# Kernel optimization log

Measured on AMD Instinct MI355X. Metric: run time of the kernel, lower is better.

## Reference

```python
import jax, jax.numpy as jnp
import numpy as np

B, S, DM, H, DH = 2, 2048, 2048, 8, 128
INNER = H * DH
ROPE_BASE = 10000.0


def setup_inputs() -> dict:
    key = jax.random.key(0)
    ks = jax.random.split(key, 8)
    sc = 0.02
    return {
        "x": jax.random.normal(ks[0], (B, S, DM), jnp.float32),
        "Wq": jax.random.normal(ks[1], (INNER, DM), jnp.float32) * sc,
        "Wk": jax.random.normal(ks[2], (INNER, DM), jnp.float32) * sc,
        "Wv": jax.random.normal(ks[3], (INNER, DM), jnp.float32) * sc,
        "Wo": jax.random.normal(ks[4], (DM, INNER), jnp.float32) * sc,
        "Wb": jax.random.normal(ks[5], (H, DM), jnp.float32) * sc,
        "bb": jax.random.normal(ks[6], (H,), jnp.float32) * sc,
        "alpha_log": -2.0 + 0.5 * jax.random.normal(ks[7], (H, DH), jnp.float32),
    }


def _rope(t):
    # cos/sin tables of shape [S, DH//2]
    inv_freq = 1.0 / (ROPE_BASE ** (jnp.arange(0, DH, 2, dtype=jnp.float32) / DH))
    freqs = jnp.arange(t, dtype=jnp.float32)[:, None] * inv_freq[None, :]
    return jnp.cos(freqs), jnp.sin(freqs)


def _apply_rotary(x, cos, sin):
    # x: [B,S,H,DH]; cos/sin: [S, DH//2] broadcast over B,H
    x1, x2 = x[..., : DH // 2], x[..., DH // 2 :]
    c = cos[None, :, None, :]
    s = sin[None, :, None, :]
    return jnp.concatenate([x1 * c - x2 * s, x2 * c + x1 * s], axis=-1)


def reference(x, Wq, Wk, Wv, Wo, Wb, bb, alpha_log):
    q = (x @ Wq.T).reshape(B, S, H, DH)
    k = (x @ Wk.T).reshape(B, S, H, DH)
    v = (x @ Wv.T).reshape(B, S, H, DH)

    cos, sin = _rope(S)
    q = _apply_rotary(q, cos, sin)
    k = _apply_rotary(k, cos, sin)

    alpha = jax.nn.sigmoid(alpha_log)                 # [H, DH]
    beta = jax.nn.sigmoid(x @ Wb.T + bb)              # [B, S, H]

    # parallel path: decayed causal linear attention
    qk = jnp.einsum("bshd,bthd->bhst", q, k)          # [B,H,S,S]
    alpha_mean = alpha.mean(axis=-1)                  # [H]
    log_alpha = jnp.log(jnp.clip(alpha_mean, 1e-6))
    pos = jnp.arange(S, dtype=jnp.float32)
    td = pos[:, None] - pos[None, :]                  # [S,S]
    decay_exp = td[None, :, :] * log_alpha[:, None, None]
    decay_exp = jnp.where(td[None, :, :] < 0, -jnp.inf, decay_exp)
    decay = jnp.exp(decay_exp)                        # [B? no: H,S,S]
    weights = qk * decay[None] * beta.transpose(0, 2, 1)[:, :, None, :]
    out = jnp.einsum("bhst,bthe->bshe", weights, v)   # [B,S,H,DH]
    output = out.reshape(B, S, INNER) @ Wo.T          # [B,S,DM]

    # accumulated state (no-grad in original): recurrent scan over time
    alpha_b = alpha[None, :, :, None]                 # [1,H,DH,1]
    kT = jnp.transpose(k, (1, 0, 2, 3))               # [S,B,H,DH]
    vT = jnp.transpose(v, (1, 0, 2, 3))
    bT = jnp.transpose(beta, (1, 0, 2))               # [S,B,H]

    def step(state, inp):
        k_t, v_t, b_t = inp
        kv = jnp.einsum("bhd,bhe->bhde", k_t, v_t)
        state = alpha_b * state + b_t[:, :, None, None] * kv
        return state, None

    state0 = jnp.zeros((B, H, DH, DH), jnp.float32)
    state, _ = jax.lax.scan(step, state0, (kT, vT, bT))
    return output, state
```

## Files before the change

kernel.cpp:

```cpp
#include <hip/hip_runtime.h>
#include <hip/hip_bf16.h>
#include <cstdint>
#include <cstddef>

#define S_LEN 2048
#define DMODEL 2048
#define NHEADS 8
#define DHEAD 128
#define INNER_DIM 1024
#define BATCH 2

typedef __bf16 bf16;
typedef __bf16 bf16x8 __attribute__((ext_vector_type(8)));
typedef __bf16 bf16x4 __attribute__((ext_vector_type(4)));
typedef float f32x4 __attribute__((ext_vector_type(4)));

#define VMCNT(n) asm volatile("s_waitcnt vmcnt(" #n ")" ::: "memory")
#define BAR()                                \
  do {                                       \
    asm volatile("" ::: "memory");           \
    __builtin_amdgcn_s_barrier();            \
    asm volatile("" ::: "memory");           \
  } while (0)

__device__ __forceinline__ void gload_lds16(const void* g, void* l) {
  __builtin_amdgcn_global_load_lds(
      (const __attribute__((address_space(1))) void*)g,
      (__attribute__((address_space(3))) void*)l, 16, 0, 0);
}

__device__ __forceinline__ float sigmoidf_(float x) {
  return 1.0f / (1.0f + expf(-x));
}

__global__ __launch_bounds__(256) void convert_w_kernel(
    const float* __restrict__ wq, const float* __restrict__ wk,
    const float* __restrict__ wv, const float* __restrict__ wo,
    bf16* __restrict__ wqkvb, bf16* __restrict__ wob) {
  size_t i4 = ((size_t)blockIdx.x * 256 + threadIdx.x) * 4;
  const float* src;
  bf16* dst;
  size_t off;
  if (i4 < 2097152UL)       { src = wq; dst = wqkvb;           off = i4; }
  else if (i4 < 4194304UL)  { src = wk; dst = wqkvb + 2097152; off = i4 - 2097152UL; }
  else if (i4 < 6291456UL)  { src = wv; dst = wqkvb + 4194304; off = i4 - 4194304UL; }
  else                      { src = wo; dst = wob;             off = i4 - 6291456UL; }
  float4 v = *(const float4*)(src + off);
  bf16x4 o;
  o[0] = (bf16)v.x; o[1] = (bf16)v.y; o[2] = (bf16)v.z; o[3] = (bf16)v.w;
  *(bf16x4*)(dst + off) = o;
}

__global__ __launch_bounds__(64) void alpha_kernel(
    const float* __restrict__ alpha_log, float* __restrict__ la_mean,
    float* __restrict__ la_d) {
  int h = blockIdx.x;
  int lane = threadIdx.x;
  float a1 = sigmoidf_(alpha_log[h * 128 + lane]);
  float a2 = sigmoidf_(alpha_log[h * 128 + 64 + lane]);
  la_d[h * 128 + lane] = logf(a1);
  la_d[h * 128 + 64 + lane] = logf(a2);
  float s = a1 + a2;
  for (int off = 32; off; off >>= 1) s += __shfl_down(s, off);
  if (lane == 0) la_mean[h] = logf(fmaxf(s * (1.0f / 128.0f), 1e-6f));
}

__global__ __launch_bounds__(64) void beta_xb_kernel(
    const float* __restrict__ x, const float* __restrict__ Wb,
    const float* __restrict__ bbias, float* __restrict__ beta,
    bf16* __restrict__ xb) {
  int n = blockIdx.x;
  int lane = threadIdx.x;
  float acc[8];
#pragma unroll
  for (int h = 0; h < 8; h++) acc[h] = 0.0f;
  const float4* x4 = (const float4*)(x + (size_t)n * DMODEL);
  bf16* xbr = xb + (size_t)n * DMODEL;
  for (int d4 = lane; d4 < DMODEL / 4; d4 += 64) {
    float4 xv = x4[d4];
    bf16x4 o;
    o[0] = (bf16)xv.x; o[1] = (bf16)xv.y; o[2] = (bf16)xv.z; o[3] = (bf16)xv.w;
    *(bf16x4*)(xbr + d4 * 4) = o;
#pragma unroll
    for (int h = 0; h < 8; h++) {
      float4 wv = ((const float4*)(Wb + (size_t)h * DMODEL))[d4];
      acc[h] += xv.x * wv.x + xv.y * wv.y + xv.z * wv.z + xv.w * wv.w;
    }
  }
#pragma unroll
  for (int off = 32; off; off >>= 1)
#pragma unroll
    for (int h = 0; h < 8; h++) acc[h] += __shfl_down(acc[h], off);
  if (lane == 0) {
#pragma unroll
    for (int h = 0; h < 8; h++)
      beta[(size_t)n * 8 + h] = sigmoidf_(acc[h] + bbias[h]);
  }
}

#define QKV_K 2048
#define QKV_NT 32

__global__ __launch_bounds__(512, 2) void qkv_gemm8p_kernel(
    const bf16* __restrict__ A, const bf16* __restrict__ Bm,
    bf16* __restrict__ C, bf16* __restrict__ vt) {
  __shared__ __align__(16) bf16 smem[2][32768];

  const int id = blockIdx.x;
  const int wg = (id & 7) * 32 + (id >> 3);
  const int tile_n = (wg >> 5) * 384;
  const int tile_m = (wg & 31) * 128;

  const int tid = threadIdx.x;
  const int lane = tid & 63;
  const int w = tid >> 6;
  const int wm = w >> 2;
  const int wn = w & 3;
  const int lr = lane & 15;
  const int kq = lane >> 4;

  const int srow = lane >> 3;
  const int slot = lane & 7;
  const int sgo = (slot ^ srow) * 8;
  const int rloc = w * 8 + srow;

  size_t Aoff[2], Boff[6];
#pragma unroll
  for (int a = 0; a < 2; ++a)
    Aoff[a] = (size_t)(tile_m + a * 64 + rloc) * QKV_K + sgo;
#pragma unroll
  for (int b = 0; b < 6; ++b) {
    const int ldsr = b * 64 + rloc;
    const int qn = ldsr >= 192 ? 1 : 0;
    const int rem = ldsr - qn * 192;
    const int wng = rem / 48;
    const int rr = rem - wng * 48;
    const int gcol = wng * 96 + qn * 48 + rr;
    Boff[b] = (size_t)(tile_n + gcol) * QKV_K + sgo;
  }

  f32x4 acc[4][6];
#pragma unroll
  for (int i = 0; i < 4; i++)
#pragma unroll
    for (int j = 0; j < 6; j++) acc[i][j] = (f32x4){0.f, 0.f, 0.f, 0.f};

  auto stageAA = [&](int buf, int k0) {
#pragma unroll
    for (int a = 0; a < 2; ++a)
      gload_lds16(A + Aoff[a] + k0, &smem[buf][(a * 64 + w * 8) * 64]);
  };
  auto stageB2 = [&](int buf, int k0, int b0) {
#pragma unroll
    for (int u = 0; u < 2; ++u)
      gload_lds16(Bm + Boff[b0 + u] + k0,
                  &smem[buf][8192 + ((b0 + u) * 64 + w * 8) * 64]);
  };

  stageAA(0, 0);
  stageB2(0, 0, 0);
  stageB2(0, 0, 2);
  stageB2(0, 0, 4);
  stageAA(1, 64);
  VMCNT(5);
  BAR();

  for (int t = 0; t < QKV_NT; ++t) {
    const int buf = t & 1;
    const int k0n = (t + 1) * 64;
    const bool h1 = (t + 1 < QKV_NT);
    const bool h2 = (t + 2 < QKV_NT);
    const bf16* ldsA = smem[buf];
    const bf16* ldsB = smem[buf] + 8192;

    bf16x8 af[2][2], b0f[3][2], b1f[3][2];

#pragma unroll
    for (int mi = 0; mi < 2; ++mi)
#pragma unroll
      for (int ks = 0; ks < 2; ++ks)
        af[mi][ks] = *(const bf16x8*)&ldsA[(wm * 64 + mi * 16 + lr) * 64 +
                                           (((ks * 4 + kq) ^ (lr & 7)) * 8)];
#pragma unroll
    for (int ni = 0; ni < 3; ++ni)
#pragma unroll
      for (int ks = 0; ks < 2; ++ks)
        b0f[ni][ks] = *(const bf16x8*)&ldsB[(wn * 48 + ni * 16 + lr) * 64 +
                                            (((ks * 4 + kq) ^ (lr & 7)) * 8)];
    if (h1) stageB2(buf ^ 1, k0n, 0);
    BAR();
    __builtin_amdgcn_s_setprio(1);
#pragma unroll
    for (int mi = 0; mi < 2; ++mi)
#pragma unroll
      for (int ni = 0; ni < 3; ++ni)
#pragma unroll
        for (int ks = 0; ks < 2; ++ks)
          acc[mi][ni] = __builtin_amdgcn_mfma_f32_16x16x32_bf16(
              af[mi][ks], b0f[ni][ks], acc[mi][ni], 0, 0, 0);
    __builtin_amdgcn_s_setprio(0);
    if (h1) VMCNT(4);
    else VMCNT(0);
    BAR();

#pragma unroll
    for (int ni = 0; ni < 3; ++ni)
#pragma unroll
      for (int ks = 0; ks < 2; ++ks)
        b1f[ni][ks] = *(const bf16x8*)&ldsB[(192 + wn * 48 + ni * 16 + lr) * 64 +
                                            (((ks * 4 + kq) ^ (lr & 7)) * 8)];
    if (h1) stageB2(buf ^ 1, k0n, 2);
    BAR();
    __builtin_amdgcn_s_setprio(1);
#pragma unroll
    for (int mi = 0; mi < 2; ++mi)
#pragma unroll
      for (int ni = 0; ni < 3; ++ni)
#pragma unroll
        for (int ks = 0; ks < 2; ++ks)
          acc[mi][3 + ni] = __builtin_amdgcn_mfma_f32_16x16x32_bf16(
              af[mi][ks], b1f[ni][ks], acc[mi][3 + ni], 0, 0, 0);
    __builtin_amdgcn_s_setprio(0);
    BAR();

#pragma unroll
    for (int mi = 0; mi < 2; ++mi)
#pragma unroll
      for (int ks = 0; ks < 2; ++ks)
        af[mi][ks] = *(const bf16x8*)&ldsA[(wm * 64 + 32 + mi * 16 + lr) * 64 +
                                           (((ks * 4 + kq) ^ (lr & 7)) * 8)];
    if (h1) stageB2(buf ^ 1, k0n, 4);
    BAR();
    __builtin_amdgcn_s_setprio(1);
#pragma unroll
    for (int mi = 0; mi < 2; ++mi)
#pragma unroll
      for (int ni = 0; ni < 3; ++ni)
#pragma unroll
        for (int ks = 0; ks < 2; ++ks)
          acc[2 + mi][3 + ni] = __builtin_amdgcn_mfma_f32_16x16x32_bf16(
              af[mi][ks], b1f[ni][ks], acc[2 + mi][3 + ni], 0, 0, 0);
    __builtin_amdgcn_s_setprio(0);
    BAR();

    if (h2) stageAA(buf, (t + 2) * 64);
    BAR();
    __builtin_amdgcn_s_setprio(1);
#pragma unroll
    for (int mi = 0; mi < 2; ++mi)
#pragma unroll
      for (int ni = 0; ni < 3; ++ni)
#pragma unroll
        for (int ks = 0; ks < 2; ++ks)
          acc[2 + mi][ni] = __builtin_amdgcn_mfma_f32_16x16x32_bf16(
              af[mi][ks], b0f[ni][ks], acc[2 + mi][ni], 0, 0, 0);
    __builtin_amdgcn_s_setprio(0);
    if (h1) {
      if (h2) VMCNT(5);
      else VMCNT(3);
    }
    BAR();
  }

  const int rb = kq * 4;
#pragma unroll
  for (int mi = 0; mi < 4; ++mi) {
    const int row0 = tile_m + wm * 64 + mi * 16 + rb;
#pragma unroll
    for (int ni = 0; ni < 6; ++ni) {
      const int col = tile_n + wn * 96 + ni * 16 + lr;
      const int z = col >> 10;
      const int cz = col & 1023;
      bf16* Cz = C + (size_t)z * 4194304UL;
#pragma unroll
      for (int r2 = 0; r2 < 4; ++r2)
        Cz[(size_t)(row0 + r2) * 1024 + cz] = (bf16)acc[mi][ni][r2];
      if (z == 2) {
        const int bb2 = row0 >> 11;
        const int ss = row0 & 2047;
        bf16x4 o4;
#pragma unroll
        for (int r2 = 0; r2 < 4; ++r2) o4[r2] = (bf16)acc[mi][ni][r2];
        *(bf16x4*)&vt[(((size_t)bb2 * 8 + (cz >> 7)) * 128 + (cz & 127)) * 2048 +
                      ss] = o4;
      }
    }
  }
}

__global__ __launch_bounds__(256) void gemm_bt_kernel(
    const bf16* __restrict__ A, const bf16* __restrict__ Bm, void* Cv, int K,
    int N, size_t strideB, size_t strideC, int obf, bf16* __restrict__ vt) {
  const int id = blockIdx.x + gridDim.x * (blockIdx.y + gridDim.y * blockIdx.z);
  const int xcd = id & 7;
  const int s = id >> 3;
  const int xs = gridDim.x >> 2;
  const int ys = gridDim.y >> 1;
  const int perz = xs * ys;
  const int z = s / perz;
  const int r = s - z * perz;
  const int tx = (xcd & 3) * xs + (r % xs);
  const int ty = (xcd >> 2) * ys + (r / xs);
  const int tile_n = tx * 128;
  const int tile_m = ty * 128;

  const bf16* Bp = Bm + (size_t)z * strideB;
  const int tid = threadIdx.x;
  const int lane = tid & 63;
  const int wv = tid >> 6;

  __shared__ bf16 As[128 * 32];
  __shared__ bf16 Bs[128 * 32];

  f32x4 acc[4][4];
#pragma unroll
  for (int i = 0; i < 4; i++)
#pragma unroll
    for (int j = 0; j < 4; j++) acc[i][j] = (f32x4){0.f, 0.f, 0.f, 0.f};

  const int wm = (wv >> 1) * 64;
  const int wn = (wv & 1) * 64;
  const int lr = lane & 15;
  const int kq = lane >> 4;
  const int swzA = ((wm + lr) >> 1) & 3;
  const int swzB = ((wn + lr) >> 1) & 3;
  const int kA = (kq ^ swzA) * 8;
  const int kB = (kq ^ swzB) * 8;

  const int ar = wv * 32 + (lane >> 2);
  const int g = ((lane & 3) ^ ((ar >> 1) & 3)) * 8;
  const bf16* Ag = A + (size_t)(tile_m + ar) * K + g;
  const bf16* Bg = Bp + (size_t)(tile_n + ar) * K + g;
  bf16* AsW = &As[wv * 1024];
  bf16* BsW = &Bs[wv * 1024];

  for (int k0 = 0; k0 < K; k0 += 32) {
    gload_lds16(Ag + k0, AsW);
    gload_lds16(Ag + (size_t)16 * K + k0, AsW + 512);
    gload_lds16(Bg + k0, BsW);
    gload_lds16(Bg + (size_t)16 * K + k0, BsW + 512);
    __syncthreads();
    bf16x8 af[4], bfr[4];
#pragma unroll
    for (int mi = 0; mi < 4; mi++)
      af[mi] = *(const bf16x8*)&As[(wm + mi * 16 + lr) * 32 + kA];
#pragma unroll
    for (int ni = 0; ni < 4; ni++)
      bfr[ni] = *(const bf16x8*)&Bs[(wn + ni * 16 + lr) * 32 + kB];
#pragma unroll
    for (int mi = 0; mi < 4; mi++)
#pragma unroll
      for (int ni = 0; ni < 4; ni++)
        acc[mi][ni] = __builtin_amdgcn_mfma_f32_16x16x32_bf16(
            af[mi], bfr[ni], acc[mi][ni], 0, 0, 0);
    __syncthreads();
  }

  const int crow0 = tile_m + wm + (lane >> 4) * 4;
  const int ccol = tile_n + wn + (lane & 15);
  if (obf) {
    bf16* Cb = (bf16*)Cv + (size_t)z * strideC;
#pragma unroll
    for (int mi = 0; mi < 4; mi++)
#pragma unroll
      for (int ni = 0; ni < 4; ni++)
#pragma unroll
        for (int r2 = 0; r2 < 4; r2++)
          Cb[(size_t)(crow0 + mi * 16 + r2) * N + ccol + ni * 16] =
              (bf16)acc[mi][ni][r2];
    if (z == 2) {
#pragma unroll
      for (int mi = 0; mi < 4; mi++) {
        int row0 = crow0 + mi * 16;
        int bb2 = row0 >> 11, ss = row0 & 2047;
#pragma unroll
        for (int ni = 0; ni < 4; ni++) {
          int col = ccol + ni * 16;
          bf16x4 o4;
#pragma unroll
          for (int r2 = 0; r2 < 4; r2++) o4[r2] = (bf16)acc[mi][ni][r2];
          *(bf16x4*)&vt[(((size_t)bb2 * 8 + (col >> 7)) * 128 + (col & 127)) *
                            2048 +
                        ss] = o4;
        }
      }
    }
  } else {
    float* Cf = (float*)Cv + (size_t)z * strideC;
#pragma unroll
    for (int mi = 0; mi < 4; mi++)
#pragma unroll
      for (int ni = 0; ni < 4; ni++)
#pragma unroll
        for (int r2 = 0; r2 < 4; r2++)
          Cf[(size_t)(crow0 + mi * 16 + r2) * N + ccol + ni * 16] =
              acc[mi][ni][r2];
  }
}

__global__ __launch_bounds__(256) void rope_kernel(bf16* __restrict__ q,
                                                   bf16* __restrict__ k) {
  int idx = blockIdx.x * 256 + threadIdx.x;
  int j0 = (idx & 15) * 4;
  int nh = idx >> 4;
  int s = (nh >> 3) & (S_LEN - 1);
  size_t base = (size_t)nh * 128 + j0;
  bf16x4 qa = *(bf16x4*)&q[base], qb = *(bf16x4*)&q[base + 64];
  bf16x4 ka = *(bf16x4*)&k[base], kb = *(bf16x4*)&k[base + 64];
#pragma unroll
  for (int jj = 0; jj < 4; jj++) {
    float inv = expf(-(float)(j0 + jj) * (9.210340371976184f / 64.0f));
    float f = (float)s * inv;
    float sn, c;
    sincosf(f, &sn, &c);
    float q1 = (float)qa[jj], q2 = (float)qb[jj];
    qa[jj] = (bf16)(q1 * c - q2 * sn);
    qb[jj] = (bf16)(q2 * c + q1 * sn);
    float k1 = (float)ka[jj], k2 = (float)kb[jj];
    ka[jj] = (bf16)(k1 * c - k2 * sn);
    kb[jj] = (bf16)(k2 * c + k1 * sn);
  }
  *(bf16x4*)&q[base] = qa;
  *(bf16x4*)&q[base + 64] = qb;
  *(bf16x4*)&k[base] = ka;
  *(bf16x4*)&k[base + 64] = kb;
}

__global__ __launch_bounds__(256) void attn_mfma_kernel(
    const bf16* __restrict__ q, const bf16* __restrict__ k,
    const bf16* __restrict__ vt, const float* __restrict__ beta,
    const float* __restrict__ la_mean, bf16* __restrict__ outb) {
  const int s0 = blockIdx.x * 64;
  const int h = blockIdx.y;
  const int b = blockIdx.z;
  const int tid = threadIdx.x;
  const int w = tid >> 6;
  const int lane = tid & 63;
  const int lr = lane & 15;
  const int kq = lane >> 4;
  const float la = la_mean[h];

  __shared__ __align__(16) bf16 Ps[4][2][16][72];

  const int sg = s0 + w * 16;
  const size_t qbase =
      ((size_t)b * S_LEN + (sg + lr)) * INNER_DIM + h * 128 + kq * 8;
  bf16x8 aq[4];
#pragma unroll
  for (int ks = 0; ks < 4; ks++)
    aq[ks] = *(const bf16x8*)&q[qbase + ks * 32];

  f32x4 O[8];
#pragma unroll
  for (int en = 0; en < 8; en++) O[en] = (f32x4){0.f, 0.f, 0.f, 0.f};

  const size_t kbase = (size_t)b * S_LEN * INNER_DIM + h * 128 + kq * 8;
  const size_t vtbase = ((size_t)b * 8 + h) * 128 * 2048;

#pragma unroll
  for (int tile = 0; tile < 2; tile++) {
    const int tb = s0 - 64 + tile * 64;
    f32x4 sc[4];
#pragma unroll
    for (int nt = 0; nt < 4; nt++) sc[nt] = (f32x4){0.f, 0.f, 0.f, 0.f};
#pragma unroll
    for (int nt = 0; nt < 4; nt++) {
      int t = tb + nt * 16 + lr;
      int tc = t > 0 ? t : 0;
#pragma unroll
      for (int ks = 0; ks < 4; ks++) {
        bf16x8 bk = *(const bf16x8*)&k[kbase + (size_t)tc * INNER_DIM + ks * 32];
        sc[nt] = __builtin_amdgcn_mfma_f32_16x16x32_bf16(aq[ks], bk, sc[nt],
                                                         0, 0, 0);
      }
    }
#pragma unroll
    for (int nt = 0; nt < 4; nt++) {
      int t = tb + nt * 16 + lr;
      int tc = t > 0 ? t : 0;
      float bt = beta[((size_t)b * S_LEN + tc) * 8 + h];
#pragma unroll
      for (int reg = 0; reg < 4; reg++) {
        int qrow = sg + kq * 4 + reg;
        int td = qrow - t;
        float wgt = 0.0f;
        if (t >= 0 && td >= 0 && td < 64)
          wgt = sc[nt][reg] * __expf((float)td * la) * bt;
        Ps[w][tile][kq * 4 + reg][nt * 16 + lr] = (bf16)wgt;
      }
    }
    __syncthreads();
    bf16x8 ap[2];
#pragma unroll
    for (int ks2 = 0; ks2 < 2; ks2++)
      ap[ks2] = *(const bf16x8*)&Ps[w][tile][lr][ks2 * 32 + kq * 8];
#pragma unroll
    for (int en = 0; en < 8; en++) {
#pragma unroll
      for (int ks2 = 0; ks2 < 2; ks2++) {
        int t0f = tb + ks2 * 32 + kq * 8;
        int tcf = t0f > 0 ? t0f : 0;
        bf16x8 bv = *(const bf16x8*)&vt[vtbase + (size_t)(en * 16 + lr) * 2048 +
                                        tcf];
        O[en] = __builtin_amdgcn_mfma_f32_16x16x32_bf16(ap[ks2], bv, O[en], 0,
                                                        0, 0);
      }
    }
  }
  const size_t obase = (size_t)b * S_LEN * INNER_DIM + h * 128;
#pragma unroll
  for (int en = 0; en < 8; en++) {
#pragma unroll
    for (int reg = 0; reg < 4; reg++) {
      int qrow = sg + kq * 4 + reg;
      outb[obase + (size_t)qrow * INNER_DIM + en * 16 + lr] =
          (bf16)O[en][reg];
    }
  }
}

__global__ __launch_bounds__(256) void state_partial_kernel(
    const bf16* __restrict__ k, const bf16* __restrict__ v,
    const float* __restrict__ beta, const float* __restrict__ la_d,
    float* __restrict__ part) {
  const int bh = blockIdx.x;
  const int chunk = blockIdx.y;
  const int b = bh >> 3, h = bh & 7;
  const int t0 = S_LEN - 512 + chunk * 32;
  const int tid = threadIdx.x;
  const int d = tid >> 1;
  const int eh = (tid & 1) * 64;

  __shared__ float ks[32][128];
  __shared__ float vsm[32][128];
  __shared__ float bs[32];

  const size_t bh_off = ((size_t)b * S_LEN) * INNER_DIM + (size_t)h * 128;
  for (int u = tid; u < 32 * 16; u += 256) {
    int r = u >> 4, c8 = (u & 15) * 8;
    bf16x8 kv = *(const bf16x8*)&k[bh_off + (size_t)(t0 + r) * INNER_DIM + c8];
    bf16x8 vv = *(const bf16x8*)&v[bh_off + (size_t)(t0 + r) * INNER_DIM + c8];
#pragma unroll
    for (int j = 0; j < 8; j++) {
      ks[r][c8 + j] = (float)kv[j];
      vsm[r][c8 + j] = (float)vv[j];
    }
  }
  if (tid < 32) bs[tid] = beta[((size_t)b * S_LEN + t0 + tid) * 8 + h];
  __syncthreads();

  const float lad = la_d[h * 128 + d];
  float acc[64];
#pragma unroll
  for (int e = 0; e < 64; e++) acc[e] = 0.0f;

  for (int tl = 0; tl < 32; tl++) {
    int m = (S_LEN - 1) - (t0 + tl);
    float f = __expf((float)m * lad);
    float coef = bs[tl] * ks[tl][d] * f;
    if (coef != 0.0f) {
#pragma unroll
      for (int e = 0; e < 64; e += 4) {
        float4 vv = *(const float4*)&vsm[tl][eh + e];
        acc[e + 0] = fmaf(coef, vv.x, acc[e + 0]);
        acc[e + 1] = fmaf(coef, vv.y, acc[e + 1]);
        acc[e + 2] = fmaf(coef, vv.z, acc[e + 2]);
        acc[e + 3] = fmaf(coef, vv.w, acc[e + 3]);
      }
    }
  }
  float* pp = part + (((size_t)chunk * 16 + bh) * 16384 + (size_t)d * 128 + eh);
#pragma unroll
  for (int e = 0; e < 64; e += 4) {
    float4 o = {acc[e + 0], acc[e + 1], acc[e + 2], acc[e + 3]};
    *(float4*)&pp[e] = o;
  }
}

__global__ __launch_bounds__(256) void state_reduce_kernel(
    const float* __restrict__ part, float* __restrict__ state) {
  size_t off = ((size_t)blockIdx.x * 256 + threadIdx.x) * 4;
  float4 s = {0.f, 0.f, 0.f, 0.f};
#pragma unroll
  for (int c = 0; c < 16; c++) {
    float4 p = *(const float4*)&part[(size_t)c * 262144 + off];
    s.x += p.x; s.y += p.y; s.z += p.z; s.w += p.w;
  }
  *(float4*)&state[off] = s;
}

extern "C" void kernel_launch(void* const* d_in, const int* in_sizes, int n_in,
                              void* d_out, int out_size, void* d_ws,
                              size_t ws_size, hipStream_t stream) {
  const float* x = (const float*)d_in[0];
  const float* Wq = (const float*)d_in[1];
  const float* Wk = (const float*)d_in[2];
  const float* Wv = (const float*)d_in[3];
  const float* Wo = (const float*)d_in[4];
  const float* Wb = (const float*)d_in[5];
  const float* bb = (const float*)d_in[6];
  const float* alog = (const float*)d_in[7];
  float* out = (float*)d_out;

  char* ws = (char*)d_ws;
  bf16* xb = (bf16*)(ws);
  float* part = (float*)(ws);
  bf16* wqkvb = (bf16*)(ws + 16777216UL);
  bf16* wob = (bf16*)(ws + 29360128UL);
  bf16* q = (bf16*)(ws + 33554432UL);
  bf16* kk = (bf16*)(ws + 41943040UL);
  bf16* vv = (bf16*)(ws + 50331648UL);
  bf16* attnb = (bf16*)(ws + 58720256UL);
  bf16* vt = (bf16*)(ws + 67108864UL);
  float* beta = (float*)(ws + 75497472UL);
  float* la_mean = (float*)(ws + 75628544UL);
  float* la_d = (float*)(ws + 75628800UL);

  convert_w_kernel<<<8192, 256, 0, stream>>>(Wq, Wk, Wv, Wo, wqkvb, wob);
  alpha_kernel<<<8, 64, 0, stream>>>(alog, la_mean, la_d);
  beta_xb_kernel<<<BATCH * S_LEN, 64, 0, stream>>>(x, Wb, bb, beta, xb);
  qkv_gemm8p_kernel<<<256, 512, 0, stream>>>(xb, wqkvb, q, vt);
  rope_kernel<<<2048, 256, 0, stream>>>(q, kk);
  attn_mfma_kernel<<<dim3(S_LEN / 64, NHEADS, BATCH), 256, 0, stream>>>(
      q, kk, vt, beta, la_mean, attnb);
  state_partial_kernel<<<dim3(16, 16), 256, 0, stream>>>(kk, vv, beta, la_d,
                                                         part);
  state_reduce_kernel<<<256, 256, 0, stream>>>(part, out + 8388608);
  gemm_bt_kernel<<<dim3(DMODEL / 128, (BATCH * S_LEN) / 128, 1), 256, 0,
                   stream>>>(attnb, wob, out, INNER_DIM, DMODEL, 0, 0, 0,
                             nullptr);
}
```

Measured before the change: 263.3 us.

## Merge prep kernels, precompute RoPE table, replace output GEMM with pipelined kernel

Folds the weight conversion, alpha, and beta/x-conversion kernels into one prep launch, which also builds a cos/sin table that the RoPE kernel now reads instead of evaluating sincos per element. The generic output-projection GEMM is replaced by a 512-thread kernel with 128x256 tiles, XOR-swizzled LDS, double buffering, and interleaved load/MFMA phases with setprio, modelled on the QKV GEMM. The aim is fewer launches and a faster output projection, at the cost of more code and a larger workspace.

```diff
diff --git a/kernel.cpp b/kernel.cpp
--- a/kernel.cpp
+++ b/kernel.cpp
@@ -33,68 +33,76 @@
   return 1.0f / (1.0f + expf(-x));
 }
 
-__global__ __launch_bounds__(256) void convert_w_kernel(
-    const float* __restrict__ wq, const float* __restrict__ wk,
-    const float* __restrict__ wv, const float* __restrict__ wo,
-    bf16* __restrict__ wqkvb, bf16* __restrict__ wob) {
-  size_t i4 = ((size_t)blockIdx.x * 256 + threadIdx.x) * 4;
-  const float* src;
-  bf16* dst;
-  size_t off;
-  if (i4 < 2097152UL)       { src = wq; dst = wqkvb;           off = i4; }
-  else if (i4 < 4194304UL)  { src = wk; dst = wqkvb + 2097152; off = i4 - 2097152UL; }
-  else if (i4 < 6291456UL)  { src = wv; dst = wqkvb + 4194304; off = i4 - 4194304UL; }
-  else                      { src = wo; dst = wob;             off = i4 - 6291456UL; }
-  float4 v = *(const float4*)(src + off);
-  bf16x4 o;
-  o[0] = (bf16)v.x; o[1] = (bf16)v.y; o[2] = (bf16)v.z; o[3] = (bf16)v.w;
-  *(bf16x4*)(dst + off) = o;
-}
-
-__global__ __launch_bounds__(64) void alpha_kernel(
-    const float* __restrict__ alpha_log, float* __restrict__ la_mean,
-    float* __restrict__ la_d) {
-  int h = blockIdx.x;
-  int lane = threadIdx.x;
-  float a1 = sigmoidf_(alpha_log[h * 128 + lane]);
-  float a2 = sigmoidf_(alpha_log[h * 128 + 64 + lane]);
-  la_d[h * 128 + lane] = logf(a1);
-  la_d[h * 128 + 64 + lane] = logf(a2);
-  float s = a1 + a2;
-  for (int off = 32; off; off >>= 1) s += __shfl_down(s, off);
-  if (lane == 0) la_mean[h] = logf(fmaxf(s * (1.0f / 128.0f), 1e-6f));
-}
-
-__global__ __launch_bounds__(64) void beta_xb_kernel(
-    const float* __restrict__ x, const float* __restrict__ Wb,
-    const float* __restrict__ bbias, float* __restrict__ beta,
-    bf16* __restrict__ xb) {
-  int n = blockIdx.x;
-  int lane = threadIdx.x;
-  float acc[8];
-#pragma unroll
-  for (int h = 0; h < 8; h++) acc[h] = 0.0f;
-  const float4* x4 = (const float4*)(x + (size_t)n * DMODEL);
-  bf16* xbr = xb + (size_t)n * DMODEL;
-  for (int d4 = lane; d4 < DMODEL / 4; d4 += 64) {
-    float4 xv = x4[d4];
+__global__ __launch_bounds__(256) void prep_kernel(
+    const float* __restrict__ x, const float* __restrict__ wq,
+    const float* __restrict__ wk, const float* __restrict__ wv,
+    const float* __restrict__ wo, const float* __restrict__ Wb,
+    const float* __restrict__ bbias, const float* __restrict__ alpha_log,
+    bf16* __restrict__ wqkvb, bf16* __restrict__ wob, bf16* __restrict__ xb,
+    float* __restrict__ beta, float* __restrict__ la_mean,
+    float* __restrict__ la_d, float2* __restrict__ cs) {
+  const int bid = blockIdx.x;
+  const int tid = threadIdx.x;
+
+  if (bid < 8192) {
+    size_t i4 = ((size_t)bid * 256 + tid) * 4;
+    const float* src;
+    bf16* dst;
+    size_t off;
+    if (i4 < 2097152UL)       { src = wq; dst = wqkvb;           off = i4; }
+    else if (i4 < 4194304UL)  { src = wk; dst = wqkvb + 2097152; off = i4 - 2097152UL; }
+    else if (i4 < 6291456UL)  { src = wv; dst = wqkvb + 4194304; off = i4 - 4194304UL; }
+    else                      { src = wo; dst = wob;             off = i4 - 6291456UL; }
+    float4 v = *(const float4*)(src + off);
     bf16x4 o;
-    o[0] = (bf16)xv.x; o[1] = (bf16)xv.y; o[2] = (bf16)xv.z; o[3] = (bf16)xv.w;
-    *(bf16x4*)(xbr + d4 * 4) = o;
-#pragma unroll
-    for (int h = 0; h < 8; h++) {
-      float4 wv = ((const float4*)(Wb + (size_t)h * DMODEL))[d4];
-      acc[h] += xv.x * wv.x + xv.y * wv.y + xv.z * wv.z + xv.w * wv.w;
-    }
-  }
-#pragma unroll
-  for (int off = 32; off; off >>= 1)
-#pragma unroll
-    for (int h = 0; h < 8; h++) acc[h] += __shfl_down(acc[h], off);
-  if (lane == 0) {
-#pragma unroll
-    for (int h = 0; h < 8; h++)
-      beta[(size_t)n * 8 + h] = sigmoidf_(acc[h] + bbias[h]);
+    o[0] = (bf16)v.x; o[1] = (bf16)v.y; o[2] = (bf16)v.z; o[3] = (bf16)v.w;
+    *(bf16x4*)(dst + off) = o;
+  } else if (bid < 9216) {
+    const int n = (bid - 8192) * 4 + (tid >> 6);
+    const int lane = tid & 63;
+    float acc[8];
+#pragma unroll
+    for (int h = 0; h < 8; h++) acc[h] = 0.0f;
+    const float4* x4 = (const float4*)(x + (size_t)n * DMODEL);
+    bf16* xbr = xb + (size_t)n * DMODEL;
+    for (int d4 = lane; d4 < DMODEL / 4; d4 += 64) {
+      float4 xv = x4[d4];
+      bf16x4 o;
+      o[0] = (bf16)xv.x; o[1] = (bf16)xv.y; o[2] = (bf16)xv.z; o[3] = (bf16)xv.w;
+      *(bf16x4*)(xbr + d4 * 4) = o;
+#pragma unroll
+      for (int h = 0; h < 8; h++) {
+        float4 wv2 = ((const float4*)(Wb + (size_t)h * DMODEL))[d4];
+        acc[h] += xv.x * wv2.x + xv.y * wv2.y + xv.z * wv2.z + xv.w * wv2.w;
+      }
+    }
+#pragma unroll
+    for (int off = 32; off; off >>= 1)
+#pragma unroll
+      for (int h = 0; h < 8; h++) acc[h] += __shfl_down(acc[h], off);
+    if (lane == 0) {
+#pragma unroll
+      for (int h = 0; h < 8; h++)
+        beta[(size_t)n * 8 + h] = sigmoidf_(acc[h] + bbias[h]);
+    }
+  } else if (bid < 9728) {
+    int idx = (bid - 9216) * 256 + tid;
+    int s = idx >> 6, j = idx & 63;
+    float f = (float)s * expf(-(float)j * (9.210340371976184f / 64.0f));
+    float sn, c;
+    sincosf(f, &sn, &c);
+    cs[idx] = make_float2(c, sn);
+  } else {
+    if (tid >= 64) return;
+    const int h = bid - 9728;
+    const int lane = tid;
+    float a1 = sigmoidf_(alpha_log[h * 128 + lane]);
+    float a2 = sigmoidf_(alpha_log[h * 128 + 64 + lane]);
+    la_d[h * 128 + lane] = logf(a1);
+    la_d[h * 128 + 64 + lane] = logf(a2);
+    float s = a1 + a2;
+    for (int off = 32; off; off >>= 1) s += __shfl_down(s, off);
+    if (lane == 0) la_mean[h] = logf(fmaxf(s * (1.0f / 128.0f), 1e-6f));
   }
 }
 
@@ -288,118 +296,185 @@
   }
 }
 
-__global__ __launch_bounds__(256) void gemm_bt_kernel(
-    const bf16* __restrict__ A, const bf16* __restrict__ Bm, void* Cv, int K,
-    int N, size_t strideB, size_t strideC, int obf, bf16* __restrict__ vt) {
-  const int id = blockIdx.x + gridDim.x * (blockIdx.y + gridDim.y * blockIdx.z);
-  const int xcd = id & 7;
-  const int s = id >> 3;
-  const int xs = gridDim.x >> 2;
-  const int ys = gridDim.y >> 1;
-  const int perz = xs * ys;
-  const int z = s / perz;
-  const int r = s - z * perz;
-  const int tx = (xcd & 3) * xs + (r % xs);
-  const int ty = (xcd >> 2) * ys + (r / xs);
-  const int tile_n = tx * 128;
-  const int tile_m = ty * 128;
-
-  const bf16* Bp = Bm + (size_t)z * strideB;
+#define OP_K 1024
+#define OP_NT 16
+
+__global__ __launch_bounds__(512, 2) void oproj_kernel(
+    const bf16* __restrict__ A, const bf16* __restrict__ Bm,
+    float* __restrict__ C) {
+  __shared__ __align__(16) bf16 smem[2][24576];
+
+  const int id = blockIdx.x;
+  const int wg = (id & 7) * 32 + (id >> 3);
+  const int tile_n = (wg >> 5) * 256;
+  const int tile_m = (wg & 31) * 128;
+
   const int tid = threadIdx.x;
   const int lane = tid & 63;
-  const int wv = tid >> 6;
-
-  __shared__ bf16 As[128 * 32];
-  __shared__ bf16 Bs[128 * 32];
-
-  f32x4 acc[4][4];
-#pragma unroll
-  for (int i = 0; i < 4; i++)
-#pragma unroll
-    for (int j = 0; j < 4; j++) acc[i][j] = (f32x4){0.f, 0.f, 0.f, 0.f};
-
-  const int wm = (wv >> 1) * 64;
-  const int wn = (wv & 1) * 64;
+  const int w = tid >> 6;
+  const int wm = w >> 2;
+  const int wn = w & 3;
   const int lr = lane & 15;
   const int kq = lane >> 4;
-  const int swzA = ((wm + lr) >> 1) & 3;
-  const int swzB = ((wn + lr) >> 1) & 3;
-  const int kA = (kq ^ swzA) * 8;
-  const int kB = (kq ^ swzB) * 8;
-
-  const int ar = wv * 32 + (lane >> 2);
-  const int g = ((lane & 3) ^ ((ar >> 1) & 3)) * 8;
-  const bf16* Ag = A + (size_t)(tile_m + ar) * K + g;
-  const bf16* Bg = Bp + (size_t)(tile_n + ar) * K + g;
-  bf16* AsW = &As[wv * 1024];
-  bf16* BsW = &Bs[wv * 1024];
-
-  for (int k0 = 0; k0 < K; k0 += 32) {
-    gload_lds16(Ag + k0, AsW);
-    gload_lds16(Ag + (size_t)16 * K + k0, AsW + 512);
-    gload_lds16(Bg + k0, BsW);
-    gload_lds16(Bg + (size_t)16 * K + k0, BsW + 512);
-    __syncthreads();
-    bf16x8 af[4], bfr[4];
-#pragma unroll
-    for (int mi = 0; mi < 4; mi++)
-      af[mi] = *(const bf16x8*)&As[(wm + mi * 16 + lr) * 32 + kA];
-#pragma unroll
-    for (int ni = 0; ni < 4; ni++)
-      bfr[ni] = *(const bf16x8*)&Bs[(wn + ni * 16 + lr) * 32 + kB];
-#pragma unroll
-    for (int mi = 0; mi < 4; mi++)
-#pragma unroll
-      for (int ni = 0; ni < 4; ni++)
-        acc[mi][ni] = __builtin_amdgcn_mfma_f32_16x16x32_bf16(
-            af[mi], bfr[ni], acc[mi][ni], 0, 0, 0);
-    __syncthreads();
-  }
-
-  const int crow0 = tile_m + wm + (lane >> 4) * 4;
-  const int ccol = tile_n + wn + (lane & 15);
-  if (obf) {
-    bf16* Cb = (bf16*)Cv + (size_t)z * strideC;
-#pragma unroll
-    for (int mi = 0; mi < 4; mi++)
-#pragma unroll
-      for (int ni = 0; ni < 4; ni++)
-#pragma unroll
-        for (int r2 = 0; r2 < 4; r2++)
-          Cb[(size_t)(crow0 + mi * 16 + r2) * N + ccol + ni * 16] =
-              (bf16)acc[mi][ni][r2];
-    if (z == 2) {
-#pragma unroll
-      for (int mi = 0; mi < 4; mi++) {
-        int row0 = crow0 + mi * 16;
-        int bb2 = row0 >> 11, ss = row0 & 2047;
-#pragma unroll
-        for (int ni = 0; ni < 4; ni++) {
-          int col = ccol + ni * 16;
-          bf16x4 o4;
-#pragma unroll
-          for (int r2 = 0; r2 < 4; r2++) o4[r2] = (bf16)acc[mi][ni][r2];
-          *(bf16x4*)&vt[(((size_t)bb2 * 8 + (col >> 7)) * 128 + (col & 127)) *
-                            2048 +
-                        ss] = o4;
-        }
-      }
-    }
-  } else {
-    float* Cf = (float*)Cv + (size_t)z * strideC;
-#pragma unroll
-    for (int mi = 0; mi < 4; mi++)
-#pragma unroll
-      for (int ni = 0; ni < 4; ni++)
-#pragma unroll
-        for (int r2 = 0; r2 < 4; r2++)
-          Cf[(size_t)(crow0 + mi * 16 + r2) * N + ccol + ni * 16] =
-              acc[mi][ni][r2];
+
+  const int srow = lane >> 3;
+  const int slot = lane & 7;
+  const int sgo = (slot ^ srow) * 8;
+  const int rloc = w * 8 + srow;
+
+  size_t Aoff[2], Boff[4];
+#pragma unroll
+  for (int a = 0; a < 2; ++a)
+    Aoff[a] = (size_t)(tile_m + a * 64 + rloc) * OP_K + sgo;
+#pragma unroll
+  for (int b = 0; b < 4; ++b) {
+    const int ldsr = b * 64 + rloc;
+    const int qn = ldsr >= 128 ? 1 : 0;
+    const int rem = ldsr - qn * 128;
+    const int wng = rem >> 5;
+    const int rr = rem & 31;
+    const int gcol = wng * 64 + qn * 32 + rr;
+    Boff[b] = (size_t)(tile_n + gcol) * OP_K + sgo;
+  }
+
+  f32x4 acc[4][4];
+#pragma unroll
+  for (int i = 0; i < 4; i++)
+#pragma unroll
+    for (int j = 0; j < 4; j++) acc[i][j] = (f32x4){0.f, 0.f, 0.f, 0.f};
+
+  auto stageAA = [&](int buf, int k0) {
+#pragma unroll
+    for (int a = 0; a < 2; ++a)
+      gload_lds16(A + Aoff[a] + k0, &smem[buf][(a * 64 + w * 8) * 64]);
+  };
+  auto stageB2 = [&](int buf, int k0, int b0) {
+#pragma unroll
+    for (int u = 0; u < 2; ++u)
+      gload_lds16(Bm + Boff[b0 + u] + k0,
+                  &smem[buf][8192 + ((b0 + u) * 64 + w * 8) * 64]);
+  };
+
+  stageAA(0, 0);
+  stageB2(0, 0, 0);
+  stageB2(0, 0, 2);
+  stageAA(1, 64);
+  VMCNT(4);
+  BAR();
+
+  for (int t = 0; t < OP_NT; ++t) {
+    const int buf = t & 1;
+    const int k0n = (t + 1) * 64;
+    const bool h1 = (t + 1 < OP_NT);
+    const bool h2 = (t + 2 < OP_NT);
+    const bf16* ldsA = smem[buf];
+    const bf16* ldsB = smem[buf] + 8192;
+
+    bf16x8 af[2][2], b0f[2][2], b1f[2][2];
+
+#pragma unroll
+    for (int mi = 0; mi < 2; ++mi)
+#pragma unroll
+      for (int ks = 0; ks < 2; ++ks)
+        af[mi][ks] = *(const bf16x8*)&ldsA[(wm * 64 + mi * 16 + lr) * 64 +
+                                           (((ks * 4 + kq) ^ (lr & 7)) * 8)];
+#pragma unroll
+    for (int ni = 0; ni < 2; ++ni)
+#pragma unroll
+      for (int ks = 0; ks < 2; ++ks)
+        b0f[ni][ks] = *(const bf16x8*)&ldsB[(wn * 32 + ni * 16 + lr) * 64 +
+                                            (((ks * 4 + kq) ^ (lr & 7)) * 8)];
+    if (h1) stageB2(buf ^ 1, k0n, 0);
+    BAR();
+    __builtin_amdgcn_s_setprio(1);
+#pragma unroll
+    for (int mi = 0; mi < 2; ++mi)
+#pragma unroll
+      for (int ni = 0; ni < 2; ++ni)
+#pragma unroll
+        for (int ks = 0; ks < 2; ++ks)
+          acc[mi][ni] = __builtin_amdgcn_mfma_f32_16x16x32_bf16(
+              af[mi][ks], b0f[ni][ks], acc[mi][ni], 0, 0, 0);
+    __builtin_amdgcn_s_setprio(0);
+    if (h1) VMCNT(4);
+    else VMCNT(0);
+    BAR();
+
+#pragma unroll
+    for (int ni = 0; ni < 2; ++ni)
+#pragma unroll
+      for (int ks = 0; ks < 2; ++ks)
+        b1f[ni][ks] = *(const bf16x8*)&ldsB[(128 + wn * 32 + ni * 16 + lr) * 64 +
+                                            (((ks * 4 + kq) ^ (lr & 7)) * 8)];
+    if (h1) stageB2(buf ^ 1, k0n, 2);
+    BAR();
+    __builtin_amdgcn_s_setprio(1);
+#pragma unroll
+    for (int mi = 0; mi < 2; ++mi)
+#pragma unroll
+      for (int ni = 0; ni < 2; ++ni)
+#pragma unroll
+        for (int ks = 0; ks < 2; ++ks)
+          acc[mi][2 + ni] = __builtin_amdgcn_mfma_f32_16x16x32_bf16(
+              af[mi][ks], b1f[ni][ks], acc[mi][2 + ni], 0, 0, 0);
+    __builtin_amdgcn_s_setprio(0);
+    BAR();
+
+#pragma unroll
+    for (int mi = 0; mi < 2; ++mi)
+#pragma unroll
+      for (int ks = 0; ks < 2; ++ks)
+        af[mi][ks] = *(const bf16x8*)&ldsA[(wm * 64 + 32 + mi * 16 + lr) * 64 +
+                                           (((ks * 4 + kq) ^ (lr & 7)) * 8)];
+    BAR();
+    __builtin_amdgcn_s_setprio(1);
+#pragma unroll
+    for (int mi = 0; mi < 2; ++mi)
+#pragma unroll
+      for (int ni = 0; ni < 2; ++ni)
+#pragma unroll
+        for (int ks = 0; ks < 2; ++ks)
+          acc[2 + mi][2 + ni] = __builtin_amdgcn_mfma_f32_16x16x32_bf16(
+              af[mi][ks], b1f[ni][ks], acc[2 + mi][2 + ni], 0, 0, 0);
+    __builtin_amdgcn_s_setprio(0);
+    BAR();
+
+    if (h2) stageAA(buf, (t + 2) * 64);
+    BAR();
+    __builtin_amdgcn_s_setprio(1);
+#pragma unroll
+    for (int mi = 0; mi < 2; ++mi)
+#pragma unroll
+      for (int ni = 0; ni < 2; ++ni)
+#pragma unroll
+        for (int ks = 0; ks < 2; ++ks)
+          acc[2 + mi][ni] = __builtin_amdgcn_mfma_f32_16x16x32_bf16(
+              af[mi][ks], b0f[ni][ks], acc[2 + mi][ni], 0, 0, 0);
+    __builtin_amdgcn_s_setprio(0);
+    if (h1) {
+      if (h2) VMCNT(4);
+      else VMCNT(2);
+    }
+    BAR();
+  }
+
+  const int rb = kq * 4;
+#pragma unroll
+  for (int i = 0; i < 4; ++i) {
+    const int row0 = tile_m + wm * 64 + (i >> 1) * 32 + (i & 1) * 16 + rb;
+#pragma unroll
+    for (int j = 0; j < 4; ++j) {
+      const int col = tile_n + wn * 64 + (j >> 1) * 32 + (j & 1) * 16 + lr;
+#pragma unroll
+      for (int r2 = 0; r2 < 4; ++r2)
+        C[(size_t)(row0 + r2) * 2048 + col] = acc[i][j][r2];
+    }
   }
 }
 
 __global__ __launch_bounds__(256) void rope_kernel(bf16* __restrict__ q,
-                                                   bf16* __restrict__ k) {
+                                                   bf16* __restrict__ k,
+                                                   const float2* __restrict__ cs) {
   int idx = blockIdx.x * 256 + threadIdx.x;
   int j0 = (idx & 15) * 4;
   int nh = idx >> 4;
@@ -407,12 +482,11 @@
   size_t base = (size_t)nh * 128 + j0;
   bf16x4 qa = *(bf16x4*)&q[base], qb = *(bf16x4*)&q[base + 64];
   bf16x4 ka = *(bf16x4*)&k[base], kb = *(bf16x4*)&k[base + 64];
+  const float2* c4 = cs + s * 64 + j0;
 #pragma unroll
   for (int jj = 0; jj < 4; jj++) {
-    float inv = expf(-(float)(j0 + jj) * (9.210340371976184f / 64.0f));
-    float f = (float)s * inv;
-    float sn, c;
-    sincosf(f, &sn, &c);
+    float c = c4[jj].x;
+    float sn = c4[jj].y;
     float q1 = (float)qa[jj], q2 = (float)qb[jj];
     qa[jj] = (bf16)(q1 * c - q2 * sn);
     qb[jj] = (bf16)(q2 * c + q1 * sn);
@@ -615,18 +689,17 @@
   float* beta = (float*)(ws + 75497472UL);
   float* la_mean = (float*)(ws + 75628544UL);
   float* la_d = (float*)(ws + 75628800UL);
-
-  convert_w_kernel<<<8192, 256, 0, stream>>>(Wq, Wk, Wv, Wo, wqkvb, wob);
-  alpha_kernel<<<8, 64, 0, stream>>>(alog, la_mean, la_d);
-  beta_xb_kernel<<<BATCH * S_LEN, 64, 0, stream>>>(x, Wb, bb, beta, xb);
+  float2* cs = (float2*)(ws + 75632896UL);
+
+  prep_kernel<<<9736, 256, 0, stream>>>(x, Wq, Wk, Wv, Wo, Wb, bb, alog,
+                                        wqkvb, wob, xb, beta, la_mean, la_d,
+                                        cs);
   qkv_gemm8p_kernel<<<256, 512, 0, stream>>>(xb, wqkvb, q, vt);
-  rope_kernel<<<2048, 256, 0, stream>>>(q, kk);
+  rope_kernel<<<2048, 256, 0, stream>>>(q, kk, cs);
   attn_mfma_kernel<<<dim3(S_LEN / 64, NHEADS, BATCH), 256, 0, stream>>>(
       q, kk, vt, beta, la_mean, attnb);
   state_partial_kernel<<<dim3(16, 16), 256, 0, stream>>>(kk, vv, beta, la_d,
                                                          part);
   state_reduce_kernel<<<256, 256, 0, stream>>>(part, out + 8388608);
-  gemm_bt_kernel<<<dim3(DMODEL / 128, (BATCH * S_LEN) / 128, 1), 256, 0,
-                   stream>>>(attnb, wob, out, INNER_DIM, DMODEL, 0, 0, 0,
-                             nullptr);
-}
+  oproj_kernel<<<256, 512, 0, stream>>>(attnb, wob, out);
+}
```

New measurement: 267.6 us. Within noise of the previous version (+1.6%).
